# Kernel tuning notes

Hardware: AMD Instinct MI355X
Metric: run time of the kernel (lower is better)

The kernel has to match this reference:

```python
import jax, jax.numpy as jnp
import numpy as np

T, B, N = 2048, 32, 1024   # time, batch, dan_hidden_size
H = 8                      # multihead_size
N2 = 128                   # attention_hidden_size
K = N // H                 # N_H = 128 per-head dim
K2 = N2 // H               # N2_H = 16 per-head attention dim


def setup_inputs() -> dict:
    key = jax.random.key(0)
    ks = jax.random.split(key, 10)
    s_n = 1.0 / np.sqrt(N)
    s_k = 1.0 / np.sqrt(K)
    s_k2 = 1.0 / np.sqrt(K2)
    return {
        "hyp": jax.random.normal(ks[0], (T, B, N), dtype=jnp.float32),
        # H independent per-head linears N -> K, stacked: (H, K, N)
        "Wmh": jax.random.uniform(ks[1], (H, K, N), minval=-s_n, maxval=s_n, dtype=jnp.float32),
        "bmh": jax.random.uniform(ks[2], (H, K), minval=-s_n, maxval=s_n, dtype=jnp.float32),
        # shared W: K -> K2
        "W": jax.random.uniform(ks[3], (K2, K), minval=-s_k, maxval=s_k, dtype=jnp.float32),
        "bW": jax.random.uniform(ks[4], (K2,), minval=-s_k, maxval=s_k, dtype=jnp.float32),
        # shared W_m: K -> K2
        "Wm": jax.random.uniform(ks[5], (K2, K), minval=-s_k, maxval=s_k, dtype=jnp.float32),
        "bWm": jax.random.uniform(ks[6], (K2,), minval=-s_k, maxval=s_k, dtype=jnp.float32),
        # shared W_h: K2 -> 1
        "Wh": jax.random.uniform(ks[7], (K2,), minval=-s_k2, maxval=s_k2, dtype=jnp.float32),
        "bWh": jax.random.uniform(ks[8], (), minval=-s_k2, maxval=s_k2, dtype=jnp.float32),
        "dan_hidden_size": N,
        "attention_hidden_size": N2,
        "multihead_size": H,
    }


def reference(hyp, Wmh, bmh, W, bW, Wm, bWm, Wh, bWh,
              dan_hidden_size, attention_hidden_size, multihead_size):
    # Per-head projections, all heads at once: (B, T, H, K)
    X = jnp.einsum('tbn,hkn->bthk', hyp, Wmh) + bmh
    # mean over time (original x.mean(0)): (B, H, K)
    m = X.mean(axis=1)
    # tanh-gated additive scoring: (B, T, H, K2)
    g = jnp.tanh(jnp.einsum('bthk,qk->bthq', X, W) + bW) \
        * jnp.tanh(jnp.einsum('bhk,qk->bhq', m, Wm) + bWm)[:, None]
    # scalar score per (b, t, h), softmax over time
    s = jnp.einsum('bthq,q->bth', g, Wh) + bWh
    a = jax.nn.softmax(s, axis=1)                       # (B, T, H)
    # attention-weighted sum over time: (B, H, K)
    c = jnp.einsum('bth,bthk->bhk', a, X)
    # concat heads along feature dim (head-major order, matches torch.cat)
    Bsz = c.shape[0]
    return c.reshape(Bsz, -1)                            # (B, N)
```

## Files before the change

kernel.cpp:

```cpp
#include <hip/hip_runtime.h>
#include <hip/hip_bf16.h>

#define T_DIM 2048
#define B_DIM 32
#define N_DIM 1024
#define H_DIM 8
#define K_DIM 128
#define Q_DIM 16

typedef __bf16 bf16x8 __attribute__((ext_vector_type(8)));
typedef __bf16 bf16x4 __attribute__((ext_vector_type(4)));
typedef float  f32x4  __attribute__((ext_vector_type(4)));

__device__ inline bf16x8 cvt8(float4 a, float4 b) {
    bf16x8 r;
    r[0] = (__bf16)a.x; r[1] = (__bf16)a.y; r[2] = (__bf16)a.z; r[3] = (__bf16)a.w;
    r[4] = (__bf16)b.x; r[5] = (__bf16)b.y; r[6] = (__bf16)b.z; r[7] = (__bf16)b.w;
    return r;
}

__global__ __launch_bounds__(256)
void cvt_f32_bf16(const float* __restrict__ s, __bf16* __restrict__ d)
{
    const long i = ((long)blockIdx.x * 256 + threadIdx.x) * 8;
    float4 a = *(const float4*)(s + i);
    float4 b = *(const float4*)(s + i + 4);
    *(bf16x8*)(d + i) = cvt8(a, b);
}

__global__ __launch_bounds__(512, 1)
void gemm_x_8ph(const __bf16* __restrict__ A, const __bf16* __restrict__ Bw,
                const float* __restrict__ bias, __bf16* __restrict__ X,
                float* __restrict__ mpart)
{
    __shared__ __bf16 ldsA[2][16384];
    __shared__ __bf16 ldsB[2][16384];
    __bf16* ldsAf = &ldsA[0][0];
    __bf16* ldsBf = &ldsB[0][0];

    const int tid  = threadIdx.x;
    const int lane = tid & 63;
    const int w    = tid >> 6;
    const int wm   = w >> 2;
    const int wn   = w & 3;

    const int bid  = blockIdx.x;
    const int wgid = (bid & 7) * 128 + (bid >> 3);
    const int bm   = wgid >> 2;
    const int bn   = wgid & 3;
    const long row0 = (long)bm * 256;
    const long col0 = (long)bn * 256;

    const int srow = w * 8 + (lane >> 3);
    const int scol = ((lane & 7) ^ (lane >> 3)) * 8;
    const __bf16* Ag = A  + (row0 + srow) * 1024 + scol;
    const __bf16* Bg = Bw + (col0 + srow) * 1024 + scol;
    const int ldst = w * 512;

    const int fr = lane & 15;
    const int g2 = lane >> 4;
    const int x7 = lane & 7;

    const __bf16* aK0 = ldsAf + (wm * 128 + fr) * 64 + ((g2    ) ^ x7) * 8;
    const __bf16* aK1 = ldsAf + (wm * 128 + fr) * 64 + ((4 + g2) ^ x7) * 8;
    const __bf16* bK0 = ldsBf + (wn * 64  + fr) * 64 + ((g2    ) ^ x7) * 8;
    const __bf16* bK1 = ldsBf + (wn * 64  + fr) * 64 + ((4 + g2) ^ x7) * 8;

    f32x4 acc[8][4];
    #pragma unroll
    for (int i = 0; i < 8; ++i)
        #pragma unroll
        for (int j = 0; j < 4; ++j)
            acc[i][j] = f32x4{0.f, 0.f, 0.f, 0.f};

    #define GLDA(SRC_, DST_) __builtin_amdgcn_global_load_lds( \
        (const __attribute__((address_space(1))) void*)(SRC_), \
        (__attribute__((address_space(3))) void*)(DST_), 16, 0, 0)

    #pragma unroll
    for (int j = 0; j < 2; ++j) GLDA(Ag + (long)j * 65536,          ldsAf + j * 4096 + ldst);
    #pragma unroll
    for (int j = 0; j < 2; ++j) GLDA(Ag + 131072 + (long)j * 65536, ldsAf + 8192 + j * 4096 + ldst);
    #pragma unroll
    for (int j = 0; j < 2; ++j) GLDA(Bg + (long)j * 65536,          ldsBf + j * 4096 + ldst);
    #pragma unroll
    for (int j = 0; j < 2; ++j) GLDA(Bg + 131072 + (long)j * 65536, ldsBf + 8192 + j * 4096 + ldst);
    #pragma unroll
    for (int j = 0; j < 2; ++j) GLDA(Bg + 64 + (long)j * 65536,          ldsBf + 16384 + j * 4096 + ldst);
    #pragma unroll
    for (int j = 0; j < 2; ++j) GLDA(Bg + 64 + 131072 + (long)j * 65536, ldsBf + 16384 + 8192 + j * 4096 + ldst);
    asm volatile("s_waitcnt vmcnt(4)" ::: "memory");
    __builtin_amdgcn_sched_barrier(0);
    __builtin_amdgcn_s_barrier();

    const __bf16* AgN = Ag + 64;
    const __bf16* BgN = Bg + 128;

    #define MFMA16(AF_, BF_, OFF_)                                             \
        __builtin_amdgcn_s_setprio(1);                                         \
        _Pragma("unroll") for (int mi = 0; mi < 4; ++mi)                       \
            _Pragma("unroll") for (int ni = 0; ni < 4; ++ni)                   \
                acc[mi + (OFF_)][ni] = __builtin_amdgcn_mfma_f32_16x16x32_bf16(\
                    BF_[ni], AF_[mi], acc[mi + (OFF_)][ni], 0, 0, 0);          \
        __builtin_amdgcn_s_setprio(0);

    #define LGKM0()                                                            \
        asm volatile("s_waitcnt lgkmcnt(0)" ::: "memory");                     \
        __builtin_amdgcn_sched_barrier(0);

    #define KTBODY(SO_, SN_, KO_, STGA_, STGB_, VM_)                           \
    {                                                                          \
        bf16x8 a0[4], b0[4], a0h[4], b1[4], a1[4], a1h[4];                     \
                   \
        _Pragma("unroll") for (int mi = 0; mi < 4; ++mi)                       \
            a0[mi] = *(const bf16x8*)(aK0 + (SO_) + mi * 1024);                \
        _Pragma("unroll") for (int ni = 0; ni < 4; ++ni)                       \
            b0[ni] = *(const bf16x8*)(bK0 + (SO_) + ni * 1024);                \
        if (STGA_) {                                                           \
            _Pragma("unroll") for (int j = 0; j < 2; ++j)                      \
                GLDA(AgN + (KO_) + (long)j * 65536,                            \
                     ldsAf + (SN_) + j * 4096 + ldst);                         \
        }                                                                      \
        __builtin_amdgcn_s_barrier();                                          \
        LGKM0();                                                               \
        MFMA16(a0, b0, 0);                                                     \
        __builtin_amdgcn_s_barrier();                                          \
                  \
        _Pragma("unroll") for (int mi = 0; mi < 4; ++mi)                       \
            a0h[mi] = *(const bf16x8*)(aK1 + (SO_) + mi * 1024);               \
        _Pragma("unroll") for (int ni = 0; ni < 4; ++ni)                       \
            b1[ni]  = *(const bf16x8*)(bK1 + (SO_) + ni * 1024);               \
        if (STGA_) {                                                           \
            _Pragma("unroll") for (int j = 0; j < 2; ++j)                      \
                GLDA(AgN + (KO_) + 131072 + (long)j * 65536,                   \
                     ldsAf + (SN_) + 8192 + j * 4096 + ldst);                  \
        }                                                                      \
        __builtin_amdgcn_s_barrier();                                          \
        LGKM0();                                                               \
        MFMA16(a0h, b1, 0);                                                    \
        __builtin_amdgcn_s_barrier();                                          \
                    \
        _Pragma("unroll") for (int mi = 0; mi < 4; ++mi)                       \
            a1[mi] = *(const bf16x8*)(aK0 + (SO_) + (mi + 4) * 1024);          \
        if (STGB_) {                                                           \
            _Pragma("unroll") for (int j = 0; j < 2; ++j)                      \
                GLDA(BgN + (KO_) + (long)j * 65536,                            \
                     ldsBf + (SO_) + j * 4096 + ldst);                         \
        }                                                                      \
        __builtin_amdgcn_s_barrier();                                          \
        LGKM0();                                                               \
        MFMA16(a1, b0, 4);                                                     \
        __builtin_amdgcn_s_barrier();                                          \
                 \
        _Pragma("unroll") for (int mi = 0; mi < 4; ++mi)                       \
            a1h[mi] = *(const bf16x8*)(aK1 + (SO_) + (mi + 4) * 1024);         \
        if (STGB_) {                                                           \
            _Pragma("unroll") for (int j = 0; j < 2; ++j)                      \
                GLDA(BgN + (KO_) + 131072 + (long)j * 65536,                   \
                     ldsBf + (SO_) + 8192 + j * 4096 + ldst);                  \
        }                                                                      \
        if ((VM_) == 4)      { asm volatile("s_waitcnt vmcnt(4)" ::: "memory"); } \
        else if ((VM_) == 0) { asm volatile("s_waitcnt vmcnt(0)" ::: "memory"); } \
        __builtin_amdgcn_sched_barrier(0);                                     \
        __builtin_amdgcn_s_barrier();                                          \
        LGKM0();                                                               \
        MFMA16(a1h, b1, 4);                                                    \
        __builtin_amdgcn_s_barrier();                                          \
    }

    #pragma unroll 1
    for (int ii = 0; ii < 7; ++ii) {
        KTBODY(0,     16384, 0,  1, 1, 4);
        KTBODY(16384, 0,     64, 1, 1, 4);
        AgN += 128; BgN += 128;
    }
    KTBODY(0,     16384, 0, 1, 0, 0);
    KTBODY(16384, 0,     0, 0, 0, -1);
    #undef KTBODY
    #undef MFMA16
    #undef LGKM0
    #undef GLDA

    const int g4 = lane >> 4;
    const long colb = col0 + wn * 64 + g4 * 4;

    float4 bias4[4];
    #pragma unroll
    for (int ni = 0; ni < 4; ++ni)
        bias4[ni] = *(const float4*)(bias + colb + ni * 16);

    f32x4 msum[2][4];
    #pragma unroll
    for (int bh = 0; bh < 2; ++bh)
        #pragma unroll
        for (int ni = 0; ni < 4; ++ni)
            msum[bh][ni] = f32x4{0.f, 0.f, 0.f, 0.f};

    #pragma unroll
    for (int mi = 0; mi < 8; ++mi) {
        const long row = row0 + wm * 128 + mi * 16 + fr;
        #pragma unroll
        for (int ni = 0; ni < 4; ++ni) {
            f32x4 xv;
            xv[0] = acc[mi][ni][0] + bias4[ni].x;
            xv[1] = acc[mi][ni][1] + bias4[ni].y;
            xv[2] = acc[mi][ni][2] + bias4[ni].z;
            xv[3] = acc[mi][ni][3] + bias4[ni].w;
            bf16x4 xb;
            xb[0] = (__bf16)xv[0]; xb[1] = (__bf16)xv[1];
            xb[2] = (__bf16)xv[2]; xb[3] = (__bf16)xv[3];
            *(bf16x4*)(X + row * 1024 + colb + ni * 16) = xb;
            msum[mi & 1][ni] += xv;
        }
    }

    float* ldsf = (float*)ldsAf;
    __syncthreads();
    if (wm == 1) {
        #pragma unroll
        for (int bh = 0; bh < 2; ++bh)
            #pragma unroll
            for (int ni = 0; ni < 4; ++ni)
                *(f32x4*)(ldsf + (bh * 16 + fr) * 256 + wn * 64 + ni * 16 + g4 * 4) = msum[bh][ni];
    }
    __syncthreads();
    if (wm == 0) {
        #pragma unroll
        for (int bh = 0; bh < 2; ++bh) {
            const int b = bh * 16 + fr;
            #pragma unroll
            for (int ni = 0; ni < 4; ++ni) {
                f32x4 other = *(const f32x4*)(ldsf + b * 256 + wn * 64 + ni * 16 + g4 * 4);
                f32x4 tot = msum[bh][ni] + other;
                *(f32x4*)(mpart + ((long)bm * 32 + b) * 1024 + colb + ni * 16) = tot;
            }
        }
    }
}

__global__ __launch_bounds__(256)
void gate2_k(const float* __restrict__ mpart, const float* __restrict__ Wm,
             const float* __restrict__ bWm, float* __restrict__ g2)
{
    __shared__ float mrow[1024];
    const int b = blockIdx.x;
    const int j4 = threadIdx.x * 4;
    f32x4 s = f32x4{0.f, 0.f, 0.f, 0.f};
    for (int bm = 0; bm < 256; ++bm)
        s += *(const f32x4*)(mpart + ((long)bm * 32 + b) * 1024 + j4);
    mrow[j4 + 0] = s[0] * (1.0f / 2048.0f);
    mrow[j4 + 1] = s[1] * (1.0f / 2048.0f);
    mrow[j4 + 2] = s[2] * (1.0f / 2048.0f);
    mrow[j4 + 3] = s[3] * (1.0f / 2048.0f);
    __syncthreads();
    if (threadIdx.x < 128) {
        const int h = threadIdx.x >> 4;
        const int q = threadIdx.x & 15;
        float d = bWm[q];
        #pragma unroll 8
        for (int k = 0; k < 128; ++k) d += mrow[h * 128 + k] * Wm[q * 128 + k];
        g2[(b * 8 + h) * 16 + q] = tanhf(d);
    }
}

__global__ __launch_bounds__(256)
void scores_k(const __bf16* __restrict__ X, const float* __restrict__ W,
              const float* __restrict__ bW, const float* __restrict__ g2,
              const float* __restrict__ Wh, const float* __restrict__ bWh,
              float* __restrict__ sbuf)
{
    const int tid   = threadIdx.x;
    const int lane  = tid & 63;
    const int w     = tid >> 6;
    const int gw    = blockIdx.x * 4 + w;
    const int rbase = gw * 16;
    const int q     = lane & 15;
    const int g4    = lane >> 4;

    bf16x8 bfr[4];
    #pragma unroll
    for (int c = 0; c < 4; ++c) {
        const float* wp = W + q * 128 + c * 32 + g4 * 8;
        float4 w0 = *(const float4*)wp;
        float4 w1 = *(const float4*)(wp + 4);
        bfr[c] = cvt8(w0, w1);
    }
    const __bf16* xp = X + (long)(rbase + q) * 128 + g4 * 8;
    bf16x8 afr[4];
    #pragma unroll
    for (int c = 0; c < 4; ++c) afr[c] = *(const bf16x8*)(xp + c * 32);

    f32x4 acc = f32x4{0.f, 0.f, 0.f, 0.f};
    #pragma unroll
    for (int c = 0; c < 4; ++c)
        acc = __builtin_amdgcn_mfma_f32_16x16x32_bf16(afr[c], bfr[c], acc, 0, 0, 0);

    const float whq  = Wh[q];
    const float bWv  = bW[q];
    const float bWhv = *bWh;
    #pragma unroll
    for (int r = 0; r < 4; ++r) {
        const int row = rbase + g4 * 4 + r;
        const int h   = row & 7;
        const int bt  = row >> 3;
        const int b   = bt & 31;
        const int t   = bt >> 5;
        float val = tanhf(acc[r] + bWv) * g2[(b * 8 + h) * 16 + q] * whq;
        val += __shfl_xor(val, 1);
        val += __shfl_xor(val, 2);
        val += __shfl_xor(val, 4);
        val += __shfl_xor(val, 8);
        if (q == 0) sbuf[(b * 8 + h) * 2048 + t] = val + bWhv;
    }
}

__global__ __launch_bounds__(256)
void softmax_k(float* __restrict__ s)
{
    __shared__ float red[256];
    const int bh = blockIdx.x;
    const int tid = threadIdx.x;
    float* row = s + bh * 2048;
    float4 v0 = *(const float4*)(row + tid * 8);
    float4 v1 = *(const float4*)(row + tid * 8 + 4);
    float v[8] = {v0.x, v0.y, v0.z, v0.w, v1.x, v1.y, v1.z, v1.w};
    float mx = v[0];
    #pragma unroll
    for (int i = 1; i < 8; ++i) mx = fmaxf(mx, v[i]);
    red[tid] = mx;
    __syncthreads();
    for (int st = 128; st > 0; st >>= 1) {
        if (tid < st) red[tid] = fmaxf(red[tid], red[tid + st]);
        __syncthreads();
    }
    mx = red[0];
    __syncthreads();
    float sum = 0.f;
    #pragma unroll
    for (int i = 0; i < 8; ++i) { v[i] = expf(v[i] - mx); sum += v[i]; }
    red[tid] = sum;
    __syncthreads();
    for (int st = 128; st > 0; st >>= 1) {
        if (tid < st) red[tid] += red[tid + st];
        __syncthreads();
    }
    const float inv = 1.0f / red[0];
    *(float4*)(row + tid * 8)     = make_float4(v[0] * inv, v[1] * inv, v[2] * inv, v[3] * inv);
    *(float4*)(row + tid * 8 + 4) = make_float4(v[4] * inv, v[5] * inv, v[6] * inv, v[7] * inv);
}

__global__ __launch_bounds__(256)
void wsum_k(const float* __restrict__ a, const __bf16* __restrict__ X,
            float* __restrict__ wpart)
{
    __shared__ float pk[8 * 128];
    const int bx = blockIdx.x;
    const int tc = bx & 7;
    const int bh = bx >> 3;
    const int b  = bh >> 3;
    const int h  = bh & 7;
    const int tid = threadIdx.x;
    const int kq = tid & 31;
    const int tr = tid >> 5;
    const float* ar = a + bh * 2048 + tc * 256;
    float a0 = 0.f, a1 = 0.f, a2 = 0.f, a3 = 0.f;
    #pragma unroll 4
    for (int i = tr; i < 256; i += 8) {
        const int t = tc * 256 + i;
        const float av = ar[i];
        bf16x4 xv = *(const bf16x4*)(X + (long)(t * 32 + b) * 1024 + h * 128 + kq * 4);
        a0 += av * (float)xv[0];
        a1 += av * (float)xv[1];
        a2 += av * (float)xv[2];
        a3 += av * (float)xv[3];
    }
    pk[tr * 128 + kq * 4 + 0] = a0;
    pk[tr * 128 + kq * 4 + 1] = a1;
    pk[tr * 128 + kq * 4 + 2] = a2;
    pk[tr * 128 + kq * 4 + 3] = a3;
    __syncthreads();
    if (tid < 128) {
        float s2 = 0.f;
        #pragma unroll
        for (int r = 0; r < 8; ++r) s2 += pk[r * 128 + tid];
        wpart[(long)bx * 128 + tid] = s2;
    }
}

__global__ __launch_bounds__(256)
void wsum_fin(const float* __restrict__ wpart, float* __restrict__ out)
{
    const int idx = blockIdx.x * 256 + threadIdx.x;
    const int k  = idx & 127;
    const int bh = idx >> 7;
    const int b  = bh >> 3;
    const int h  = bh & 7;
    float s = 0.f;
    #pragma unroll
    for (int tc = 0; tc < 8; ++tc) s += wpart[(bh * 8 + tc) * 128 + k];
    out[b * 1024 + h * 128 + k] = s;
}

extern "C" void kernel_launch(void* const* d_in, const int* in_sizes, int n_in,
                              void* d_out, int out_size, void* d_ws, size_t ws_size,
                              hipStream_t stream)
{
    const float* hyp = (const float*)d_in[0];
    const float* Wmh = (const float*)d_in[1];
    const float* bmh = (const float*)d_in[2];
    const float* W   = (const float*)d_in[3];
    const float* bW  = (const float*)d_in[4];
    const float* Wm  = (const float*)d_in[5];
    const float* bWm = (const float*)d_in[6];
    const float* Wh  = (const float*)d_in[7];
    const float* bWh = (const float*)d_in[8];
    float* out = (float*)d_out;

    char* ws = (char*)d_ws;
    const size_t SZ_X   = 134217728;
    const size_t SZ_AB  = 134217728;
    const size_t SZ_BB  = 2097152;
    const size_t SZ_MP  = 33554432;
    const size_t SZ_G2  = 16384;
    const size_t SZ_SB  = 2097152;

    size_t off = 0;
    __bf16* X     = (__bf16*)(ws + off); off += SZ_X;
    __bf16* Ab    = (__bf16*)(ws + off); off += SZ_AB;
    __bf16* Bb    = (__bf16*)(ws + off); off += SZ_BB;
    float*  mpart = (float*) (ws + off); off += SZ_MP;
    float*  g2    = (float*) (ws + off); off += SZ_G2;
    float*  sbuf  = (float*) (ws + off); off += SZ_SB;
    float*  wpart = (float*) (ws + off);

    cvt_f32_bf16<<<32768, 256, 0, stream>>>(hyp, Ab);
    cvt_f32_bf16<<<512,   256, 0, stream>>>(Wmh, Bb);
    gemm_x_8ph<<<1024, 512, 0, stream>>>(Ab, Bb, bmh, X, mpart);
    gate2_k<<<32, 256, 0, stream>>>(mpart, Wm, bWm, g2);
    scores_k<<<8192, 256, 0, stream>>>(X, W, bW, g2, Wh, bWh, sbuf);
    softmax_k<<<256, 256, 0, stream>>>(sbuf);
    wsum_k<<<2048, 256, 0, stream>>>(sbuf, X, wpart);
    wsum_fin<<<128, 256, 0, stream>>>(wpart, out);
}
```

Baseline: 328.4 us.

## Fuse fp32-to-bf16 conversion of activations into GEMM A-tile staging

Drops the separate conversion pass over the 256MB fp32 activation tensor. The GEMM now loads fp32 A tiles into registers, converts them to bf16 and writes them to LDS, prefetching one k-step ahead, in place of async global-to-LDS copies of a pre-converted bf16 copy. This removes a full read/write pass and the bf16 staging buffer. In exchange the GEMM reads twice as many A bytes, needs more registers, and adjusts its vmcnt waits to fit the new pipeline.

```diff
diff --git a/kernel.cpp b/kernel.cpp
--- a/kernel.cpp
+++ b/kernel.cpp
@@ -29,7 +29,7 @@
 }
 
 __global__ __launch_bounds__(512, 1)
-void gemm_x_8ph(const __bf16* __restrict__ A, const __bf16* __restrict__ Bw,
+void gemm_x_8ph(const float* __restrict__ A, const __bf16* __restrict__ Bw,
                 const float* __restrict__ bias, __bf16* __restrict__ X,
                 float* __restrict__ mpart)
 {
@@ -53,9 +53,10 @@
 
     const int srow = w * 8 + (lane >> 3);
     const int scol = ((lane & 7) ^ (lane >> 3)) * 8;
-    const __bf16* Ag = A  + (row0 + srow) * 1024 + scol;
+    const float*  Af = A  + (row0 + srow) * 1024 + scol;
     const __bf16* Bg = Bw + (col0 + srow) * 1024 + scol;
     const int ldst = w * 512;
+    __bf16* ldsAw = ldsAf + ldst + (lane & 63) * 8;
 
     const int fr = lane & 15;
     const int g2 = lane >> 4;
@@ -77,23 +78,36 @@
         (const __attribute__((address_space(1))) void*)(SRC_), \
         (__attribute__((address_space(3))) void*)(DST_), 16, 0, 0)
 
-    #pragma unroll
-    for (int j = 0; j < 2; ++j) GLDA(Ag + (long)j * 65536,          ldsAf + j * 4096 + ldst);
-    #pragma unroll
-    for (int j = 0; j < 2; ++j) GLDA(Ag + 131072 + (long)j * 65536, ldsAf + 8192 + j * 4096 + ldst);
-    #pragma unroll
-    for (int j = 0; j < 2; ++j) GLDA(Bg + (long)j * 65536,          ldsBf + j * 4096 + ldst);
-    #pragma unroll
-    for (int j = 0; j < 2; ++j) GLDA(Bg + 131072 + (long)j * 65536, ldsBf + 8192 + j * 4096 + ldst);
+    float4 rA[8];
+    #pragma unroll
+    for (int j = 0; j < 4; ++j) {
+        rA[2*j]   = *(const float4*)(Af + (long)j * 65536);
+        rA[2*j+1] = *(const float4*)(Af + (long)j * 65536 + 4);
+    }
+    #pragma unroll
+    for (int j = 0; j < 2; ++j) GLDA(Bg + (long)j * 65536,               ldsBf + j * 4096 + ldst);
+    #pragma unroll
+    for (int j = 0; j < 2; ++j) GLDA(Bg + 131072 + (long)j * 65536,      ldsBf + 8192 + j * 4096 + ldst);
     #pragma unroll
     for (int j = 0; j < 2; ++j) GLDA(Bg + 64 + (long)j * 65536,          ldsBf + 16384 + j * 4096 + ldst);
     #pragma unroll
     for (int j = 0; j < 2; ++j) GLDA(Bg + 64 + 131072 + (long)j * 65536, ldsBf + 16384 + 8192 + j * 4096 + ldst);
-    asm volatile("s_waitcnt vmcnt(4)" ::: "memory");
+    *(bf16x8*)(ldsAw        ) = cvt8(rA[0], rA[1]);
+    *(bf16x8*)(ldsAw +  4096) = cvt8(rA[2], rA[3]);
+    *(bf16x8*)(ldsAw +  8192) = cvt8(rA[4], rA[5]);
+    *(bf16x8*)(ldsAw + 12288) = cvt8(rA[6], rA[7]);
+    #pragma unroll
+    for (int j = 0; j < 4; ++j) {
+        rA[2*j]   = *(const float4*)(Af + 64 + (long)j * 65536);
+        rA[2*j+1] = *(const float4*)(Af + 64 + (long)j * 65536 + 4);
+    }
+    asm volatile("s_waitcnt vmcnt(12)" ::: "memory");
+    __builtin_amdgcn_sched_barrier(0);
+    asm volatile("s_waitcnt lgkmcnt(0)" ::: "memory");
     __builtin_amdgcn_sched_barrier(0);
     __builtin_amdgcn_s_barrier();
 
-    const __bf16* AgN = Ag + 64;
+    const float*  AfN = Af + 128;
     const __bf16* BgN = Bg + 128;
 
     #define MFMA16(AF_, BF_, OFF_)                                             \
@@ -108,38 +122,40 @@
         asm volatile("s_waitcnt lgkmcnt(0)" ::: "memory");                     \
         __builtin_amdgcn_sched_barrier(0);
 
-    #define KTBODY(SO_, SN_, KO_, STGA_, STGB_, VM_)                           \
+    #define KTBODY(SO_, SN_, KO_, STGAW_, STGAL_, STGB_, VM_)                  \
     {                                                                          \
         bf16x8 a0[4], b0[4], a0h[4], b1[4], a1[4], a1h[4];                     \
-                   \
+                      \
         _Pragma("unroll") for (int mi = 0; mi < 4; ++mi)                       \
             a0[mi] = *(const bf16x8*)(aK0 + (SO_) + mi * 1024);                \
         _Pragma("unroll") for (int ni = 0; ni < 4; ++ni)                       \
             b0[ni] = *(const bf16x8*)(bK0 + (SO_) + ni * 1024);                \
-        if (STGA_) {                                                           \
-            _Pragma("unroll") for (int j = 0; j < 2; ++j)                      \
-                GLDA(AgN + (KO_) + (long)j * 65536,                            \
-                     ldsAf + (SN_) + j * 4096 + ldst);                         \
+        if (STGAW_) {                                                          \
+            *(bf16x8*)(ldsAw + (SN_)        ) = cvt8(rA[0], rA[1]);            \
+            *(bf16x8*)(ldsAw + (SN_) +  4096) = cvt8(rA[2], rA[3]);            \
+            *(bf16x8*)(ldsAw + (SN_) +  8192) = cvt8(rA[4], rA[5]);            \
+            *(bf16x8*)(ldsAw + (SN_) + 12288) = cvt8(rA[6], rA[7]);            \
+        }                                                                      \
+        if (STGAL_) {                                                          \
+            _Pragma("unroll") for (int j = 0; j < 4; ++j) {                    \
+                rA[2*j]   = *(const float4*)(AfN + (KO_) + (long)j * 65536);   \
+                rA[2*j+1] = *(const float4*)(AfN + (KO_) + (long)j * 65536 + 4);\
+            }                                                                  \
         }                                                                      \
         __builtin_amdgcn_s_barrier();                                          \
         LGKM0();                                                               \
         MFMA16(a0, b0, 0);                                                     \
         __builtin_amdgcn_s_barrier();                                          \
-                  \
+                                                         \
         _Pragma("unroll") for (int mi = 0; mi < 4; ++mi)                       \
             a0h[mi] = *(const bf16x8*)(aK1 + (SO_) + mi * 1024);               \
         _Pragma("unroll") for (int ni = 0; ni < 4; ++ni)                       \
             b1[ni]  = *(const bf16x8*)(bK1 + (SO_) + ni * 1024);               \
-        if (STGA_) {                                                           \
-            _Pragma("unroll") for (int j = 0; j < 2; ++j)                      \
-                GLDA(AgN + (KO_) + 131072 + (long)j * 65536,                   \
-                     ldsAf + (SN_) + 8192 + j * 4096 + ldst);                  \
-        }                                                                      \
         __builtin_amdgcn_s_barrier();                                          \
         LGKM0();                                                               \
         MFMA16(a0h, b1, 0);                                                    \
         __builtin_amdgcn_s_barrier();                                          \
-                    \
+                             \
         _Pragma("unroll") for (int mi = 0; mi < 4; ++mi)                       \
             a1[mi] = *(const bf16x8*)(aK0 + (SO_) + (mi + 4) * 1024);          \
         if (STGB_) {                                                           \
@@ -151,7 +167,7 @@
         LGKM0();                                                               \
         MFMA16(a1, b0, 4);                                                     \
         __builtin_amdgcn_s_barrier();                                          \
-                 \
+                          \
         _Pragma("unroll") for (int mi = 0; mi < 4; ++mi)                       \
             a1h[mi] = *(const bf16x8*)(aK1 + (SO_) + (mi + 4) * 1024);         \
         if (STGB_) {                                                           \
@@ -159,8 +175,8 @@
                 GLDA(BgN + (KO_) + 131072 + (long)j * 65536,                   \
                      ldsBf + (SO_) + 8192 + j * 4096 + ldst);                  \
         }                                                                      \
-        if ((VM_) == 4)      { asm volatile("s_waitcnt vmcnt(4)" ::: "memory"); } \
-        else if ((VM_) == 0) { asm volatile("s_waitcnt vmcnt(0)" ::: "memory"); } \
+        if ((VM_) == 12)     { asm volatile("s_waitcnt vmcnt(12)" ::: "memory"); } \
+        else if ((VM_) == 0) { asm volatile("s_waitcnt vmcnt(0)" ::: "memory"); }  \
         __builtin_amdgcn_sched_barrier(0);                                     \
         __builtin_amdgcn_s_barrier();                                          \
         LGKM0();                                                               \
@@ -170,12 +186,12 @@
 
     #pragma unroll 1
     for (int ii = 0; ii < 7; ++ii) {
-        KTBODY(0,     16384, 0,  1, 1, 4);
-        KTBODY(16384, 0,     64, 1, 1, 4);
-        AgN += 128; BgN += 128;
-    }
-    KTBODY(0,     16384, 0, 1, 0, 0);
-    KTBODY(16384, 0,     0, 0, 0, -1);
+        KTBODY(0,     16384, 0,  1, 1, 1, 12);
+        KTBODY(16384, 0,     64, 1, 1, 1, 12);
+        AfN += 128; BgN += 128;
+    }
+    KTBODY(0,     16384, 0, 1, 0, 0, 0);
+    KTBODY(16384, 0,     0, 0, 0, 0, -1);
     #undef KTBODY
     #undef MFMA16
     #undef LGKM0
@@ -418,7 +434,6 @@
 
     char* ws = (char*)d_ws;
     const size_t SZ_X   = 134217728;
-    const size_t SZ_AB  = 134217728;
     const size_t SZ_BB  = 2097152;
     const size_t SZ_MP  = 33554432;
     const size_t SZ_G2  = 16384;
@@ -426,16 +441,14 @@
 
     size_t off = 0;
     __bf16* X     = (__bf16*)(ws + off); off += SZ_X;
-    __bf16* Ab    = (__bf16*)(ws + off); off += SZ_AB;
     __bf16* Bb    = (__bf16*)(ws + off); off += SZ_BB;
     float*  mpart = (float*) (ws + off); off += SZ_MP;
     float*  g2    = (float*) (ws + off); off += SZ_G2;
     float*  sbuf  = (float*) (ws + off); off += SZ_SB;
     float*  wpart = (float*) (ws + off);
 
-    cvt_f32_bf16<<<32768, 256, 0, stream>>>(hyp, Ab);
-    cvt_f32_bf16<<<512,   256, 0, stream>>>(Wmh, Bb);
-    gemm_x_8ph<<<1024, 512, 0, stream>>>(Ab, Bb, bmh, X, mpart);
+    cvt_f32_bf16<<<512, 256, 0, stream>>>(Wmh, Bb);
+    gemm_x_8ph<<<1024, 512, 0, stream>>>(hyp, Bb, bmh, X, mpart);
     gate2_k<<<32, 256, 0, stream>>>(mpart, Wm, bWm, g2);
     scores_k<<<8192, 256, 0, stream>>>(X, W, bW, g2, Wh, bWh, sbuf);
     softmax_k<<<256, 256, 0, stream>>>(sbuf);
```

Result: slower. 335.9 us (+2.3%).

## Fuse scoring, softmax and weighted sum into one online-softmax attention kernel

Applied to the files above, without the earlier changes.

Replaces the four tail kernels (scores, softmax, weighted sum, final reduction) with a single kernel per (batch, head) that computes scores in 64-step time chunks. It keeps a running max and sum (online softmax) and rescales the accumulated context as it goes. This removes the score buffer round trip and three launches. It also drops bWh, which cancels in the softmax. The catch is that only 256 blocks run, each looping serially over 32 chunks with several barriers per chunk, so parallelism is lower and the X re-read becomes a serial per-block stream.

```diff
diff --git a/kernel.cpp b/kernel.cpp
--- a/kernel.cpp
+++ b/kernel.cpp
@@ -111,7 +111,6 @@
     #define KTBODY(SO_, SN_, KO_, STGA_, STGB_, VM_)                           \
     {                                                                          \
         bf16x8 a0[4], b0[4], a0h[4], b1[4], a1[4], a1h[4];                     \
-                   \
         _Pragma("unroll") for (int mi = 0; mi < 4; ++mi)                       \
             a0[mi] = *(const bf16x8*)(aK0 + (SO_) + mi * 1024);                \
         _Pragma("unroll") for (int ni = 0; ni < 4; ++ni)                       \
@@ -125,7 +124,6 @@
         LGKM0();                                                               \
         MFMA16(a0, b0, 0);                                                     \
         __builtin_amdgcn_s_barrier();                                          \
-                  \
         _Pragma("unroll") for (int mi = 0; mi < 4; ++mi)                       \
             a0h[mi] = *(const bf16x8*)(aK1 + (SO_) + mi * 1024);               \
         _Pragma("unroll") for (int ni = 0; ni < 4; ++ni)                       \
@@ -139,7 +137,6 @@
         LGKM0();                                                               \
         MFMA16(a0h, b1, 0);                                                    \
         __builtin_amdgcn_s_barrier();                                          \
-                    \
         _Pragma("unroll") for (int mi = 0; mi < 4; ++mi)                       \
             a1[mi] = *(const bf16x8*)(aK0 + (SO_) + (mi + 4) * 1024);          \
         if (STGB_) {                                                           \
@@ -151,7 +148,6 @@
         LGKM0();                                                               \
         MFMA16(a1, b0, 4);                                                     \
         __builtin_amdgcn_s_barrier();                                          \
-                 \
         _Pragma("unroll") for (int mi = 0; mi < 4; ++mi)                       \
             a1h[mi] = *(const bf16x8*)(aK1 + (SO_) + (mi + 4) * 1024);         \
         if (STGB_) {                                                           \
@@ -264,18 +260,25 @@
 }
 
 __global__ __launch_bounds__(256)
-void scores_k(const __bf16* __restrict__ X, const float* __restrict__ W,
-              const float* __restrict__ bW, const float* __restrict__ g2,
-              const float* __restrict__ Wh, const float* __restrict__ bWh,
-              float* __restrict__ sbuf)
+void attn_k(const __bf16* __restrict__ X, const float* __restrict__ W,
+            const float* __restrict__ bW, const float* __restrict__ g2,
+            const float* __restrict__ Wh, float* __restrict__ out)
 {
-    const int tid   = threadIdx.x;
-    const int lane  = tid & 63;
-    const int w     = tid >> 6;
-    const int gw    = blockIdx.x * 4 + w;
-    const int rbase = gw * 16;
-    const int q     = lane & 15;
-    const int g4    = lane >> 4;
+    __shared__ float sch[64];
+    __shared__ float pl[64];
+    __shared__ float red[1024];
+    __shared__ float scal[3];
+
+    const int tid  = threadIdx.x;
+    const int lane = tid & 63;
+    const int w    = tid >> 6;
+    const int bh   = blockIdx.x;
+    const int b    = bh >> 3;
+    const int h    = bh & 7;
+    const int q    = lane & 15;
+    const int g4   = lane >> 4;
+
+    if (tid == 0) { scal[0] = -1e30f; scal[1] = 0.f; scal[2] = 0.f; }
 
     bf16x8 bfr[4];
     #pragma unroll
@@ -285,120 +288,90 @@
         float4 w1 = *(const float4*)(wp + 4);
         bfr[c] = cvt8(w0, w1);
     }
-    const __bf16* xp = X + (long)(rbase + q) * 128 + g4 * 8;
-    bf16x8 afr[4];
-    #pragma unroll
-    for (int c = 0; c < 4; ++c) afr[c] = *(const bf16x8*)(xp + c * 32);
-
-    f32x4 acc = f32x4{0.f, 0.f, 0.f, 0.f};
-    #pragma unroll
-    for (int c = 0; c < 4; ++c)
-        acc = __builtin_amdgcn_mfma_f32_16x16x32_bf16(afr[c], bfr[c], acc, 0, 0, 0);
-
-    const float whq  = Wh[q];
-    const float bWv  = bW[q];
-    const float bWhv = *bWh;
-    #pragma unroll
-    for (int r = 0; r < 4; ++r) {
-        const int row = rbase + g4 * 4 + r;
-        const int h   = row & 7;
-        const int bt  = row >> 3;
-        const int b   = bt & 31;
-        const int t   = bt >> 5;
-        float val = tanhf(acc[r] + bWv) * g2[(b * 8 + h) * 16 + q] * whq;
-        val += __shfl_xor(val, 1);
-        val += __shfl_xor(val, 2);
-        val += __shfl_xor(val, 4);
-        val += __shfl_xor(val, 8);
-        if (q == 0) sbuf[(b * 8 + h) * 2048 + t] = val + bWhv;
-    }
-}
-
-__global__ __launch_bounds__(256)
-void softmax_k(float* __restrict__ s)
-{
-    __shared__ float red[256];
-    const int bh = blockIdx.x;
-    const int tid = threadIdx.x;
-    float* row = s + bh * 2048;
-    float4 v0 = *(const float4*)(row + tid * 8);
-    float4 v1 = *(const float4*)(row + tid * 8 + 4);
-    float v[8] = {v0.x, v0.y, v0.z, v0.w, v1.x, v1.y, v1.z, v1.w};
-    float mx = v[0];
-    #pragma unroll
-    for (int i = 1; i < 8; ++i) mx = fmaxf(mx, v[i]);
-    red[tid] = mx;
+    const float whq = Wh[q];
+    const float bWv = bW[q];
+    const float gq  = g2[(b * 8 + h) * 16 + q];
+
+    const __bf16* xp = X + ((long)(w * 16 + q) * 32 + b) * 1024 + h * 128 + g4 * 8;
+    const int tr = tid >> 5;
+    const int kq = tid & 31;
+    const __bf16* xa = X + ((long)tr * 32 + b) * 1024 + h * 128 + kq * 4;
+
+    float c0 = 0.f, c1 = 0.f, c2 = 0.f, c3 = 0.f;
+
     __syncthreads();
-    for (int st = 128; st > 0; st >>= 1) {
-        if (tid < st) red[tid] = fmaxf(red[tid], red[tid + st]);
+
+    #pragma unroll 1
+    for (int ch = 0; ch < 32; ++ch) {
+        bf16x8 afr[4];
+        #pragma unroll
+        for (int c = 0; c < 4; ++c) afr[c] = *(const bf16x8*)(xp + c * 32);
+        f32x4 acc = f32x4{0.f, 0.f, 0.f, 0.f};
+        #pragma unroll
+        for (int c = 0; c < 4; ++c)
+            acc = __builtin_amdgcn_mfma_f32_16x16x32_bf16(afr[c], bfr[c], acc, 0, 0, 0);
+        #pragma unroll
+        for (int r = 0; r < 4; ++r) {
+            float val = tanhf(acc[r] + bWv) * gq * whq;
+            val += __shfl_xor(val, 1);
+            val += __shfl_xor(val, 2);
+            val += __shfl_xor(val, 4);
+            val += __shfl_xor(val, 8);
+            if (q == 0) sch[w * 16 + g4 * 4 + r] = val;
+        }
         __syncthreads();
-    }
-    mx = red[0];
-    __syncthreads();
-    float sum = 0.f;
-    #pragma unroll
-    for (int i = 0; i < 8; ++i) { v[i] = expf(v[i] - mx); sum += v[i]; }
-    red[tid] = sum;
-    __syncthreads();
-    for (int st = 128; st > 0; st >>= 1) {
-        if (tid < st) red[tid] += red[tid + st];
+
+        if (tid < 64) {
+            float v = sch[tid];
+            float mx = v;
+            #pragma unroll
+            for (int off = 1; off < 64; off <<= 1)
+                mx = fmaxf(mx, __shfl_xor(mx, off));
+            const float mold = scal[0];
+            const float newm = fmaxf(mold, mx);
+            const float f    = __expf(mold - newm);
+            const float p    = __expf(v - newm);
+            pl[tid] = p;
+            float ps = p;
+            #pragma unroll
+            for (int off = 1; off < 64; off <<= 1)
+                ps += __shfl_xor(ps, off);
+            if (tid == 0) {
+                scal[0] = newm;
+                scal[1] = f;
+                scal[2] = scal[2] * f + ps;
+            }
+        }
         __syncthreads();
-    }
-    const float inv = 1.0f / red[0];
-    *(float4*)(row + tid * 8)     = make_float4(v[0] * inv, v[1] * inv, v[2] * inv, v[3] * inv);
-    *(float4*)(row + tid * 8 + 4) = make_float4(v[4] * inv, v[5] * inv, v[6] * inv, v[7] * inv);
-}
-
-__global__ __launch_bounds__(256)
-void wsum_k(const float* __restrict__ a, const __bf16* __restrict__ X,
-            float* __restrict__ wpart)
-{
-    __shared__ float pk[8 * 128];
-    const int bx = blockIdx.x;
-    const int tc = bx & 7;
-    const int bh = bx >> 3;
-    const int b  = bh >> 3;
-    const int h  = bh & 7;
-    const int tid = threadIdx.x;
-    const int kq = tid & 31;
-    const int tr = tid >> 5;
-    const float* ar = a + bh * 2048 + tc * 256;
-    float a0 = 0.f, a1 = 0.f, a2 = 0.f, a3 = 0.f;
-    #pragma unroll 4
-    for (int i = tr; i < 256; i += 8) {
-        const int t = tc * 256 + i;
-        const float av = ar[i];
-        bf16x4 xv = *(const bf16x4*)(X + (long)(t * 32 + b) * 1024 + h * 128 + kq * 4);
-        a0 += av * (float)xv[0];
-        a1 += av * (float)xv[1];
-        a2 += av * (float)xv[2];
-        a3 += av * (float)xv[3];
-    }
-    pk[tr * 128 + kq * 4 + 0] = a0;
-    pk[tr * 128 + kq * 4 + 1] = a1;
-    pk[tr * 128 + kq * 4 + 2] = a2;
-    pk[tr * 128 + kq * 4 + 3] = a3;
+
+        const float f = scal[1];
+        if (f != 1.0f) { c0 *= f; c1 *= f; c2 *= f; c3 *= f; }
+        #pragma unroll
+        for (int i = 0; i < 8; ++i) {
+            const float p = pl[tr + 8 * i];
+            bf16x4 xv = *(const bf16x4*)(xa + (long)(8 * i) * 32768);
+            c0 += p * (float)xv[0];
+            c1 += p * (float)xv[1];
+            c2 += p * (float)xv[2];
+            c3 += p * (float)xv[3];
+        }
+        __syncthreads();
+
+        xp += 64 * 32768;
+        xa += 64 * 32768;
+    }
+
+    red[tr * 128 + kq * 4 + 0] = c0;
+    red[tr * 128 + kq * 4 + 1] = c1;
+    red[tr * 128 + kq * 4 + 2] = c2;
+    red[tr * 128 + kq * 4 + 3] = c3;
     __syncthreads();
     if (tid < 128) {
-        float s2 = 0.f;
-        #pragma unroll
-        for (int r = 0; r < 8; ++r) s2 += pk[r * 128 + tid];
-        wpart[(long)bx * 128 + tid] = s2;
-    }
-}
-
-__global__ __launch_bounds__(256)
-void wsum_fin(const float* __restrict__ wpart, float* __restrict__ out)
-{
-    const int idx = blockIdx.x * 256 + threadIdx.x;
-    const int k  = idx & 127;
-    const int bh = idx >> 7;
-    const int b  = bh >> 3;
-    const int h  = bh & 7;
-    float s = 0.f;
-    #pragma unroll
-    for (int tc = 0; tc < 8; ++tc) s += wpart[(bh * 8 + tc) * 128 + k];
-    out[b * 1024 + h * 128 + k] = s;
+        float s = 0.f;
+        #pragma unroll
+        for (int r = 0; r < 8; ++r) s += red[r * 128 + tid];
+        out[b * 1024 + h * 128 + tid] = s / scal[2];
+    }
 }
 
 extern "C" void kernel_launch(void* const* d_in, const int* in_sizes, int n_in,
@@ -413,7 +386,6 @@
     const float* Wm  = (const float*)d_in[5];
     const float* bWm = (const float*)d_in[6];
     const float* Wh  = (const float*)d_in[7];
-    const float* bWh = (const float*)d_in[8];
     float* out = (float*)d_out;
 
     char* ws = (char*)d_ws;
@@ -422,7 +394,6 @@
     const size_t SZ_BB  = 2097152;
     const size_t SZ_MP  = 33554432;
     const size_t SZ_G2  = 16384;
-    const size_t SZ_SB  = 2097152;
 
     size_t off = 0;
     __bf16* X     = (__bf16*)(ws + off); off += SZ_X;
@@ -430,15 +401,10 @@
     __bf16* Bb    = (__bf16*)(ws + off); off += SZ_BB;
     float*  mpart = (float*) (ws + off); off += SZ_MP;
     float*  g2    = (float*) (ws + off); off += SZ_G2;
-    float*  sbuf  = (float*) (ws + off); off += SZ_SB;
-    float*  wpart = (float*) (ws + off);
 
     cvt_f32_bf16<<<32768, 256, 0, stream>>>(hyp, Ab);
     cvt_f32_bf16<<<512,   256, 0, stream>>>(Wmh, Bb);
     gemm_x_8ph<<<1024, 512, 0, stream>>>(Ab, Bb, bmh, X, mpart);
     gate2_k<<<32, 256, 0, stream>>>(mpart, Wm, bWm, g2);
-    scores_k<<<8192, 256, 0, stream>>>(X, W, bW, g2, Wh, bWh, sbuf);
-    softmax_k<<<256, 256, 0, stream>>>(sbuf);
-    wsum_k<<<2048, 256, 0, stream>>>(sbuf, X, wpart);
-    wsum_fin<<<128, 256, 0, stream>>>(wpart, out);
-}
+    attn_k<<<256, 256, 0, stream>>>(X, W, bW, g2, Wh, out);
+}
```

Measured after the change: 340.0 us. 1.04x slower.
